# Optimization experiments

Hardware: AMD Instinct MI355X
Metric: run time of the kernel (lower is better)

## Reference

```python
import jax, jax.numpy as jnp
import numpy as np

# --- LIF neuron (spikingjelly LIFNode, single-step, tau=2.0, hard reset, ATan surrogate) ---
# With zero initial membrane potential, one step gives h = x / tau, spike = heaviside(h - v_th).
ALPHA = 2.0  # ATan surrogate default alpha
TAU = 2.0    # LIFNode default tau
V_TH = 1.0

@jax.custom_vjp
def atan_heaviside(x):
    return (x >= 0.0).astype(x.dtype)

def _ah_fwd(x):
    return (x >= 0.0).astype(x.dtype), x

def _ah_bwd(res, g):
    # d/dx of ATan surrogate: alpha / (2 * (1 + (pi/2 * alpha * x)^2))
    return (g * (ALPHA / (2.0 * (1.0 + (jnp.pi / 2.0 * ALPHA * res) ** 2))),)

atan_heaviside.defvjp(_ah_fwd, _ah_bwd)

def lif(x):
    return atan_heaviside(x / TAU - V_TH)

DIM, NUM_HEADS, TOPK = 256, 8, 4
WT, WH, WW = 2, 4, 4

def setup_inputs() -> dict:
    key = jax.random.key(0)
    k1, k2, k3, k4, k5 = jax.random.split(key, 5)
    T, B, Lt, Lh, Lw, C = 4, 2, 8, 32, 32, DIM
    x = jax.random.normal(k1, (T, B, Lt, Lh, Lw, C), dtype=jnp.float32)
    w_qkv = jax.random.normal(k2, (C, 3 * C), dtype=jnp.float32) * 0.02
    b_qkv = jax.random.normal(k3, (3 * C,), dtype=jnp.float32) * 0.02
    w_proj = jax.random.normal(k4, (C, C), dtype=jnp.float32) * 0.02
    b_proj = jax.random.normal(k5, (C,), dtype=jnp.float32) * 0.02
    return {"x": x, "w_qkv": w_qkv, "b_qkv": b_qkv, "w_proj": w_proj, "b_proj": b_proj}

def reference(x, w_qkv, b_qkv, w_proj, b_proj):
    T, B, Lt, Lh, Lw, C = x.shape
    H = NUM_HEADS
    D = C // H
    scale = D ** -0.5
    lt, lh, lw = Lt // WT, Lh // WH, Lw // WW
    W = WT * WH * WW          # num_wins = 32
    S = lt * lh * lw          # win_size = 256

    # window partition: [T,B,Lt,Lh,Lw,C] -> [T,B,W,S,C]
    xw = x.reshape(T, B, WT, lt, WH, lh, WW, lw, C)
    xw = xw.transpose(0, 1, 2, 4, 6, 3, 5, 7, 8).reshape(T, B, W, S, C)

    # region routing: mean over timesteps and tokens -> [B,W,C]
    region = xw.mean(axis=(0, 3))
    scores = jnp.einsum('bwc,bvc->bwv', region, region) * scale  # [B,W,W]
    idx = jax.lax.top_k(scores, TOPK)[1]                          # [B,W,K] int32

    # qkv projection + spiking activations
    qkv = xw @ w_qkv + b_qkv                                      # [T,B,W,S,3C]
    q, k, v = jnp.split(qkv, 3, axis=-1)
    q, k, v = lif(q), lif(k), lif(v)
    q = q.reshape(T, B, W, S, H, D)
    k = k.reshape(T, B, W, S, H, D)
    v = v.reshape(T, B, W, S, H, D)

    # gather routed KV blocks: k_g[t,b,w,j] = k[t,b,idx[b,w,j]]
    b_ix = jnp.arange(B)[:, None, None]
    k_g = k[:, b_ix, idx].reshape(T, B, W, TOPK * S, H, D)        # [T,B,W,K*S,H,D]
    v_g = v[:, b_ix, idx].reshape(T, B, W, TOPK * S, H, D)

    # linear attention: kv = k^T v, out = q @ kv, normalized by q @ sum(k)
    kv = jnp.einsum('tbwnhd,tbwnhe->tbwhde', k_g, v_g)            # [T,B,W,H,D,D]
    out = jnp.einsum('tbwshd,tbwhde->tbwshe', q, kv)              # [T,B,W,S,H,D]
    den = jnp.einsum('tbwshd,tbwhd->tbwsh', q, k_g.sum(axis=3))[..., None]
    out = out / (den + 1e-6)

    out = out.reshape(T, B, W, S, C) @ w_proj + b_proj

    # window reverse: [T,B,W,S,C] -> [T,B,Lt,Lh,Lw,C]
    out = out.reshape(T, B, WT, WH, WW, lt, lh, lw, C)
    out = out.transpose(0, 1, 2, 5, 3, 6, 4, 7, 8).reshape(T, B, Lt, Lh, Lw, C)
    return out
```

## Files before the change

### kernel.cpp

```cpp
#include <hip/hip_runtime.h>
#include <hip/hip_bf16.h>
#include <stdint.h>

#define NT 4
#define NB 2
#define NW 32
#define NS 256
#define NC 256
#define NH 8
#define ND 32
#define NK 4

#define LDP 40

typedef unsigned int u32;
typedef unsigned short u16;
typedef __attribute__((ext_vector_type(8))) short bf16x8;
typedef __attribute__((ext_vector_type(8))) unsigned short u16x8;
typedef __attribute__((ext_vector_type(4))) float f32x4;

__device__ __forceinline__ int wofs(int w) {
  return (w >> 4) * 4096 + ((w >> 2) & 3) * 256 + (w & 3) * 8;
}
__device__ __forceinline__ int sofs(int s) {
  return ((s >> 6) << 10) + (((s >> 3) & 7) << 5) + (s & 7);
}
__device__ __forceinline__ size_t x_off(int t, int b, int w, int s, int c) {
  return ((size_t)((t * NB + b) * 8192 + wofs(w) + sofs(s))) * NC + c;
}

__device__ __forceinline__ u32 f2bf(float f) {
  union { float f; u32 i; } u; u.f = f;
  return (u.i + 0x7FFFu + ((u.i >> 16) & 1u)) >> 16;
}

__global__ __launch_bounds__(256) void k_convw(const float* __restrict__ w_qkv,
                                               u16* __restrict__ bt) {
  int i = blockIdx.x * 256 + threadIdx.x;
  int k = i / 768, n = i % 768;
  bt[(size_t)n * 256 + k] = (u16)f2bf(w_qkv[i]);
}

__global__ __launch_bounds__(256) void k_gemm(const float* __restrict__ x,
                                              const u16* __restrict__ bt,
                                              const float* __restrict__ b_qkv,
                                              u32* __restrict__ qb, u32* __restrict__ kb,
                                              u32* __restrict__ vb,
                                              float* __restrict__ partial,
                                              u32* __restrict__ winflag) {
  __shared__ __align__(16) u16 As[2][128 * LDP];
  __shared__ __align__(16) u16 Bs[2][128 * LDP];
  __shared__ u32 pack[128 * 4];
  __shared__ float4 sums4[2][256];
  __shared__ u32 wfl;

  const int tid = threadIdx.x;
  const int v = (blockIdx.x & 7) * 384 + (blockIdx.x >> 3);
  const int mt = v / 6, nt = v % 6;
  const int m0 = mt * 128, n0 = nt * 128;
  const int wave = tid >> 6, lane = tid & 63;
  const int wr = wave >> 1, wc = wave & 1;
  const bool doreg = (nt == 0);

  if (tid == 0) wfl = 0;
  for (int i = tid; i < 128 * 4; i += 256) pack[i] = 0;

  const f32x4 vz = {0.f, 0.f, 0.f, 0.f};
  f32x4 acc[4][4];
#pragma unroll
  for (int m = 0; m < 4; ++m)
#pragma unroll
    for (int n = 0; n < 4; ++n) acc[m][n] = vz;

  auto stage = [&](int buf, int ks) {
    const int k0 = ks * 32;
    const int r0 = tid >> 3, c4 = tid & 7;
    float4 sv = {0.f, 0.f, 0.f, 0.f};
#pragma unroll
    for (int p = 0; p < 4; ++p) {
      int row = p * 32 + r0;
      float4 vx = *reinterpret_cast<const float4*>(&x[(size_t)(m0 + row) * NC + k0 + c4 * 4]);
      sv.x += vx.x; sv.y += vx.y; sv.z += vx.z; sv.w += vx.w;
      uint2 bf;
      bf.x = f2bf(vx.x) | (f2bf(vx.y) << 16);
      bf.y = f2bf(vx.z) | (f2bf(vx.w) << 16);
      *reinterpret_cast<uint2*>(&As[buf][row * LDP + c4 * 4]) = bf;
    }
    if (doreg) sums4[ks & 1][tid] = sv;
#pragma unroll
    for (int p = 0; p < 2; ++p) {
      int idx2 = p * 256 + tid;
      int row = idx2 >> 2, ch = idx2 & 3;
      u16x8 vbb = *reinterpret_cast<const u16x8*>(&bt[(size_t)(n0 + row) * 256 + k0 + ch * 8]);
      *reinterpret_cast<u16x8*>(&Bs[buf][row * LDP + ch * 8]) = vbb;
    }
  };

  stage(0, 0);
  __syncthreads();
#pragma unroll
  for (int ks = 0; ks < 8; ++ks) {
    const int buf = ks & 1;
    if (doreg && (tid >> 5) == ks) {
      int local = tid & 31, c4l = local >> 2, comp = local & 3;
      const float* sp = reinterpret_cast<const float*>(&sums4[ks & 1][0]);
#pragma unroll
      for (int ww = 0; ww < 4; ++ww) {
        float s = 0.f;
#pragma unroll
        for (int j = 0; j < 8; ++j) s += sp[((ww * 8 + j) * 8 + c4l) * 4 + comp];
        partial[((size_t)mt * 4 + ww) * NC + tid] = s;
      }
    }
    if (ks < 7) stage(buf ^ 1, ks + 1);
    bf16x8 afr[4], bfr[4];
#pragma unroll
    for (int m = 0; m < 4; ++m)
      afr[m] = *reinterpret_cast<const bf16x8*>(
          &As[buf][(wr * 64 + m * 16 + (lane & 15)) * LDP + (lane >> 4) * 8]);
#pragma unroll
    for (int n = 0; n < 4; ++n)
      bfr[n] = *reinterpret_cast<const bf16x8*>(
          &Bs[buf][(wc * 64 + n * 16 + (lane & 15)) * LDP + (lane >> 4) * 8]);
#pragma unroll
    for (int m = 0; m < 4; ++m)
#pragma unroll
      for (int n = 0; n < 4; ++n)
        acc[m][n] = __builtin_amdgcn_mfma_f32_16x16x32_bf16(afr[m], bfr[n], acc[m][n], 0, 0, 0);
    __syncthreads();
  }

  float bias[4];
#pragma unroll
  for (int n = 0; n < 4; ++n) bias[n] = b_qkv[n0 + wc * 64 + n * 16 + (lane & 15)];
#pragma unroll
  for (int m = 0; m < 4; ++m)
#pragma unroll
    for (int n = 0; n < 4; ++n)
#pragma unroll
      for (int r = 0; r < 4; ++r) {
        float vv = acc[m][n][r] + bias[n];
        if (vv >= 2.0f) {
          int row = wr * 64 + m * 16 + (lane >> 4) * 4 + r;
          int colb = wc * 64 + n * 16 + (lane & 15);
          atomicOr(&pack[row * 4 + (colb >> 5)], 1u << (colb & 31));
        }
      }
  __syncthreads();
  u32* dst = (nt < 2) ? qb : (nt < 4) ? kb : vb;
  const int h0 = (nt * 4) & 7;
  u32 anyb = 0;
  for (int i = tid; i < 128 * 4; i += 256) {
    int row = i >> 2, j = i & 3;
    u32 pv = pack[i];
    dst[(size_t)(m0 + row) * NH + h0 + j] = pv;
    if (pv) anyb |= 1u << ((row & 31) >> 3);
  }
  if (anyb) atomicOr(&wfl, anyb);
  __syncthreads();
  if (tid == 0 && wfl) {
    int t = mt >> 7, b = (mt >> 6) & 1, Lt = (mt >> 3) & 7, hh = mt & 7;
    int w0 = (Lt >> 2) * 16 + (hh >> 1) * 4;
    u32 bit = (nt < 2) ? 1u : (nt < 4) ? 2u : 4u;
    for (int ww = 0; ww < 4; ++ww)
      if (wfl & (1u << ww))
        atomicOr(&winflag[(t * NB + b) * NW + w0 + ww], bit);
  }
}

__global__ __launch_bounds__(256) void k_reduce(const float* __restrict__ partial,
                                                float* __restrict__ region) {
  int blk = blockIdx.x;
  int b = blk >> 5, v = blk & 31;
  int c = threadIdx.x;
  int wt = v >> 4, wh = (v >> 2) & 3, ww = v & 3;
  float s = 0.f;
#pragma unroll
  for (int t = 0; t < NT; ++t)
#pragma unroll
    for (int it = 0; it < 4; ++it)
#pragma unroll
      for (int hl = 0; hl < 2; ++hl) {
        int m = ((t * NB + b) * 8 + wt * 4 + it) * 8 + (wh * 2 + hl);
        s += partial[((size_t)m * 4 + ww) * NC + c];
      }
  region[(size_t)blk * NC + c] = s * (1.0f / 1024.0f);
}

__global__ __launch_bounds__(256) void k_scores(const float* __restrict__ region,
                                                int* __restrict__ idx) {
  __shared__ float rs[NW][NC];
  __shared__ float scval[NW];
  int blk = blockIdx.x;
  int b = blk >> 5, w = blk & 31;
  int tid = threadIdx.x;
  for (int i = tid; i < NW * NC; i += 256)
    rs[i >> 8][i & 255] = region[(size_t)b * NW * NC + i];
  __syncthreads();
  int v = tid >> 3, l8 = tid & 7;
  float sum = 0.f;
  const float* a = rs[w];
  const float* bb = rs[v];
#pragma unroll
  for (int j = 0; j < 32; ++j) sum += a[l8 * 32 + j] * bb[l8 * 32 + j];
  sum += __shfl_xor(sum, 1);
  sum += __shfl_xor(sum, 2);
  sum += __shfl_xor(sum, 4);
  if (l8 == 0) scval[v] = sum * 0.17677669529663687f;
  __syncthreads();
  if (tid == 0) {
    float sc[NW];
#pragma unroll
    for (int j = 0; j < NW; ++j) sc[j] = scval[j];
    for (int kk = 0; kk < NK; ++kk) {
      float best = -__builtin_inff(); int bi = 0;
      for (int j = 0; j < NW; ++j)
        if (sc[j] > best) { best = sc[j]; bi = j; }
      idx[(b * NW + w) * NK + kk] = bi;
      sc[bi] = -__builtin_inff();
    }
  }
}

__global__ __launch_bounds__(256) void k_attn(const u32* __restrict__ qb,
                                              const u32* __restrict__ kb,
                                              const u32* __restrict__ vb,
                                              const int* __restrict__ idx,
                                              const u32* __restrict__ winflag,
                                              const float* __restrict__ w_proj,
                                              const float* __restrict__ b_proj,
                                              float* __restrict__ out) {
  __shared__ u32 qs[NS * NH];
  __shared__ unsigned short kvc[NH * ND * ND];
  __shared__ u32 ksum[NH * ND];
  __shared__ float attnrow[NC];

  int blk = blockIdx.x;
  int t = blk >> 6, b = (blk >> 5) & 1, w = blk & 31;
  int tid = threadIdx.x;

  u32 fs = winflag[(t * NB + b) * NW + w];
  int wj[NK];
  u32 fk = 0, fv = 0;
#pragma unroll
  for (int j = 0; j < NK; ++j) {
    wj[j] = idx[(b * NW + w) * NK + j];
    u32 f = winflag[(t * NB + b) * NW + wj[j]];
    fk |= f & 2u; fv |= f & 4u;
  }
  bool skip = !(fs & 1u) || !fk || !fv;

  if (skip) {
    float bp = b_proj[tid];
    for (int s = 0; s < NS; ++s) out[x_off(t, b, w, s, tid)] = bp;
    return;
  }

  int tb = (t * NB + b) * 8192;
  size_t gb[NK];
#pragma unroll
  for (int j = 0; j < NK; ++j) gb[j] = (size_t)(tb + wofs(wj[j])) * NH;
  size_t qbase = (size_t)(tb + wofs(w)) * NH;
  for (int i = tid; i < NS * NH; i += 256)
    qs[i] = qb[qbase + (size_t)sofs(i >> 3) * NH + (i & 7)];
  {
    int h = tid >> 5, d = tid & 31;
    u32 cnt = 0;
    for (int n = 0; n < NK * NS; ++n)
      cnt += (kb[gb[n >> 8] + (size_t)sofs(n & 255) * NH + h] >> d) & 1u;
    ksum[tid] = cnt;
  }
  for (int p = tid; p < NH * ND * ND; p += 256) {
    int h = p >> 10, d = (p >> 5) & 31, e = p & 31;
    u32 cnt = 0;
    for (int n = 0; n < NK * NS; ++n) {
      size_t a = gb[n >> 8] + (size_t)sofs(n & 255) * NH + h;
      cnt += ((kb[a] >> d) & (vb[a] >> e)) & 1u;
    }
    kvc[p] = (unsigned short)cnt;
  }
  __syncthreads();
  int h = tid >> 5, e = tid & 31;
  float bpv = b_proj[tid];
  for (int s = 0; s < NS; ++s) {
    u32 qw = qs[s * NH + h];
    float num = 0.f, den = 0.f;
    for (int d = 0; d < ND; ++d) {
      if ((qw >> d) & 1u) {
        den += (float)ksum[h * ND + d];
        num += (float)kvc[h * ND * ND + d * ND + e];
      }
    }
    attnrow[tid] = num / (den + 1e-6f);
    __syncthreads();
    float acc = bpv;
    for (int c = 0; c < NC; ++c) acc += attnrow[c] * w_proj[c * NC + tid];
    out[x_off(t, b, w, s, tid)] = acc;
    __syncthreads();
  }
}

extern "C" void kernel_launch(void* const* d_in, const int* in_sizes, int n_in,
                              void* d_out, int out_size, void* d_ws, size_t ws_size,
                              hipStream_t stream) {
  const float* x      = (const float*)d_in[0];
  const float* w_qkv  = (const float*)d_in[1];
  const float* b_qkv  = (const float*)d_in[2];
  const float* w_proj = (const float*)d_in[3];
  const float* b_proj = (const float*)d_in[4];
  float* out = (float*)d_out;

  char* ws = (char*)d_ws;
  float* partial = (float*)ws;
  int* idx       = (int*)(ws + 0x200000);
  u16* bt        = (u16*)(ws + 0x201000);
  u32* winflag   = (u32*)(ws + 0x280000);
  float* region  = (float*)(ws + 0x290000);
  u32* qb        = (u32*)(ws + 0x300000);
  u32* kb        = qb + (size_t)NT * NB * NW * NS * NH;
  u32* vb        = kb + (size_t)NT * NB * NW * NS * NH;

  hipMemsetAsync(winflag, 0, NT * NB * NW * sizeof(u32), stream);
  k_convw<<<768, 256, 0, stream>>>(w_qkv, bt);
  k_gemm<<<3072, 256, 0, stream>>>(x, bt, b_qkv, qb, kb, vb, partial, winflag);
  k_reduce<<<NB * NW, 256, 0, stream>>>(partial, region);
  k_scores<<<NB * NW, 256, 0, stream>>>(region, idx);
  k_attn<<<NT * NB * NW, 256, 0, stream>>>(qb, kb, vb, idx, winflag, w_proj, b_proj, out);
}
```

Before: 81.93 us.

## Pre-convert x to bf16, use direct global-to-LDS loads, split attention blocks by tokens

```diff
diff --git a/kernel.cpp b/kernel.cpp
--- a/kernel.cpp
+++ b/kernel.cpp
@@ -11,12 +11,9 @@
 #define ND 32
 #define NK 4
 
-#define LDP 40
-
 typedef unsigned int u32;
 typedef unsigned short u16;
 typedef __attribute__((ext_vector_type(8))) short bf16x8;
-typedef __attribute__((ext_vector_type(8))) unsigned short u16x8;
 typedef __attribute__((ext_vector_type(4))) float f32x4;
 
 __device__ __forceinline__ int wofs(int w) {
@@ -32,6 +29,12 @@
 __device__ __forceinline__ u32 f2bf(float f) {
   union { float f; u32 i; } u; u.f = f;
   return (u.i + 0x7FFFu + ((u.i >> 16) & 1u)) >> 16;
+}
+
+__device__ __forceinline__ void gload16(const u16* g, u16* l) {
+  __builtin_amdgcn_global_load_lds(
+      (const __attribute__((address_space(1))) void*)g,
+      (__attribute__((address_space(3))) void*)l, 16, 0, 0);
 }
 
 __global__ __launch_bounds__(256) void k_convw(const float* __restrict__ w_qkv,
@@ -41,131 +44,37 @@
   bt[(size_t)n * 256 + k] = (u16)f2bf(w_qkv[i]);
 }
 
-__global__ __launch_bounds__(256) void k_gemm(const float* __restrict__ x,
-                                              const u16* __restrict__ bt,
-                                              const float* __restrict__ b_qkv,
-                                              u32* __restrict__ qb, u32* __restrict__ kb,
-                                              u32* __restrict__ vb,
-                                              float* __restrict__ partial,
-                                              u32* __restrict__ winflag) {
-  __shared__ __align__(16) u16 As[2][128 * LDP];
-  __shared__ __align__(16) u16 Bs[2][128 * LDP];
-  __shared__ u32 pack[128 * 4];
-  __shared__ float4 sums4[2][256];
-  __shared__ u32 wfl;
-
-  const int tid = threadIdx.x;
-  const int v = (blockIdx.x & 7) * 384 + (blockIdx.x >> 3);
-  const int mt = v / 6, nt = v % 6;
-  const int m0 = mt * 128, n0 = nt * 128;
-  const int wave = tid >> 6, lane = tid & 63;
-  const int wr = wave >> 1, wc = wave & 1;
-  const bool doreg = (nt == 0);
-
-  if (tid == 0) wfl = 0;
-  for (int i = tid; i < 128 * 4; i += 256) pack[i] = 0;
-
-  const f32x4 vz = {0.f, 0.f, 0.f, 0.f};
-  f32x4 acc[4][4];
-#pragma unroll
-  for (int m = 0; m < 4; ++m)
-#pragma unroll
-    for (int n = 0; n < 4; ++n) acc[m][n] = vz;
-
-  auto stage = [&](int buf, int ks) {
-    const int k0 = ks * 32;
-    const int r0 = tid >> 3, c4 = tid & 7;
-    float4 sv = {0.f, 0.f, 0.f, 0.f};
-#pragma unroll
-    for (int p = 0; p < 4; ++p) {
-      int row = p * 32 + r0;
-      float4 vx = *reinterpret_cast<const float4*>(&x[(size_t)(m0 + row) * NC + k0 + c4 * 4]);
-      sv.x += vx.x; sv.y += vx.y; sv.z += vx.z; sv.w += vx.w;
-      uint2 bf;
-      bf.x = f2bf(vx.x) | (f2bf(vx.y) << 16);
-      bf.y = f2bf(vx.z) | (f2bf(vx.w) << 16);
-      *reinterpret_cast<uint2*>(&As[buf][row * LDP + c4 * 4]) = bf;
-    }
-    if (doreg) sums4[ks & 1][tid] = sv;
-#pragma unroll
-    for (int p = 0; p < 2; ++p) {
-      int idx2 = p * 256 + tid;
-      int row = idx2 >> 2, ch = idx2 & 3;
-      u16x8 vbb = *reinterpret_cast<const u16x8*>(&bt[(size_t)(n0 + row) * 256 + k0 + ch * 8]);
-      *reinterpret_cast<u16x8*>(&Bs[buf][row * LDP + ch * 8]) = vbb;
-    }
-  };
-
-  stage(0, 0);
-  __syncthreads();
-#pragma unroll
-  for (int ks = 0; ks < 8; ++ks) {
-    const int buf = ks & 1;
-    if (doreg && (tid >> 5) == ks) {
-      int local = tid & 31, c4l = local >> 2, comp = local & 3;
-      const float* sp = reinterpret_cast<const float*>(&sums4[ks & 1][0]);
-#pragma unroll
-      for (int ww = 0; ww < 4; ++ww) {
-        float s = 0.f;
-#pragma unroll
-        for (int j = 0; j < 8; ++j) s += sp[((ww * 8 + j) * 8 + c4l) * 4 + comp];
-        partial[((size_t)mt * 4 + ww) * NC + tid] = s;
-      }
-    }
-    if (ks < 7) stage(buf ^ 1, ks + 1);
-    bf16x8 afr[4], bfr[4];
-#pragma unroll
-    for (int m = 0; m < 4; ++m)
-      afr[m] = *reinterpret_cast<const bf16x8*>(
-          &As[buf][(wr * 64 + m * 16 + (lane & 15)) * LDP + (lane >> 4) * 8]);
-#pragma unroll
-    for (int n = 0; n < 4; ++n)
-      bfr[n] = *reinterpret_cast<const bf16x8*>(
-          &Bs[buf][(wc * 64 + n * 16 + (lane & 15)) * LDP + (lane >> 4) * 8]);
-#pragma unroll
-    for (int m = 0; m < 4; ++m)
-#pragma unroll
-      for (int n = 0; n < 4; ++n)
-        acc[m][n] = __builtin_amdgcn_mfma_f32_16x16x32_bf16(afr[m], bfr[n], acc[m][n], 0, 0, 0);
-    __syncthreads();
-  }
-
-  float bias[4];
-#pragma unroll
-  for (int n = 0; n < 4; ++n) bias[n] = b_qkv[n0 + wc * 64 + n * 16 + (lane & 15)];
-#pragma unroll
-  for (int m = 0; m < 4; ++m)
-#pragma unroll
-    for (int n = 0; n < 4; ++n)
-#pragma unroll
-      for (int r = 0; r < 4; ++r) {
-        float vv = acc[m][n][r] + bias[n];
-        if (vv >= 2.0f) {
-          int row = wr * 64 + m * 16 + (lane >> 4) * 4 + r;
-          int colb = wc * 64 + n * 16 + (lane & 15);
-          atomicOr(&pack[row * 4 + (colb >> 5)], 1u << (colb & 31));
-        }
-      }
-  __syncthreads();
-  u32* dst = (nt < 2) ? qb : (nt < 4) ? kb : vb;
-  const int h0 = (nt * 4) & 7;
-  u32 anyb = 0;
-  for (int i = tid; i < 128 * 4; i += 256) {
-    int row = i >> 2, j = i & 3;
-    u32 pv = pack[i];
-    dst[(size_t)(m0 + row) * NH + h0 + j] = pv;
-    if (pv) anyb |= 1u << ((row & 31) >> 3);
-  }
-  if (anyb) atomicOr(&wfl, anyb);
-  __syncthreads();
-  if (tid == 0 && wfl) {
-    int t = mt >> 7, b = (mt >> 6) & 1, Lt = (mt >> 3) & 7, hh = mt & 7;
-    int w0 = (Lt >> 2) * 16 + (hh >> 1) * 4;
-    u32 bit = (nt < 2) ? 1u : (nt < 4) ? 2u : 4u;
-    for (int ww = 0; ww < 4; ++ww)
-      if (wfl & (1u << ww))
-        atomicOr(&winflag[(t * NB + b) * NW + w0 + ww], bit);
-  }
+__global__ __launch_bounds__(256) void k_convx(const float* __restrict__ x,
+                                               u16* __restrict__ xw,
+                                               float* __restrict__ partial) {
+  __shared__ float sums[4][4][NC];
+  int blk = blockIdx.x;
+  int tid = threadIdx.x;
+  int g = tid >> 6, c4 = tid & 63;
+  size_t base = (size_t)blk * 128;
+  float4 s[4];
+#pragma unroll
+  for (int ww = 0; ww < 4; ++ww) s[ww] = make_float4(0.f, 0.f, 0.f, 0.f);
+#pragma unroll
+  for (int p = 0; p < 32; ++p) {
+    int row = p * 4 + g;
+    float4 v = *reinterpret_cast<const float4*>(&x[(base + row) * NC + c4 * 4]);
+    uint2 bf;
+    bf.x = f2bf(v.x) | (f2bf(v.y) << 16);
+    bf.y = f2bf(v.z) | (f2bf(v.w) << 16);
+    *reinterpret_cast<uint2*>(&xw[(base + row) * NC + c4 * 4]) = bf;
+    int ww = (p & 7) >> 1;
+    s[ww].x += v.x; s[ww].y += v.y; s[ww].z += v.z; s[ww].w += v.w;
+  }
+#pragma unroll
+  for (int ww = 0; ww < 4; ++ww)
+    *reinterpret_cast<float4*>(&sums[ww][g][c4 * 4]) = s[ww];
+  __syncthreads();
+  int c = tid;
+#pragma unroll
+  for (int ww = 0; ww < 4; ++ww)
+    partial[((size_t)blk * 4 + ww) * NC + c] =
+        sums[ww][0][c] + sums[ww][1][c] + sums[ww][2][c] + sums[ww][3][c];
 }
 
 __global__ __launch_bounds__(256) void k_reduce(const float* __restrict__ partial,
@@ -180,9 +89,9 @@
 #pragma unroll
     for (int it = 0; it < 4; ++it)
 #pragma unroll
-      for (int hl = 0; hl < 2; ++hl) {
-        int m = ((t * NB + b) * 8 + wt * 4 + it) * 8 + (wh * 2 + hl);
-        s += partial[((size_t)m * 4 + ww) * NC + c];
+      for (int j = 0; j < 2; ++j) {
+        int pb = (t * NB + b) * 64 + (wt * 4 + it) * 8 + (wh * 2 + j);
+        s += partial[((size_t)pb * 4 + ww) * NC + c];
       }
   region[(size_t)blk * NC + c] = s * (1.0f / 1024.0f);
 }
@@ -222,6 +131,107 @@
   }
 }
 
+__global__ __launch_bounds__(256) void k_gemm(const u16* __restrict__ xw,
+                                              const u16* __restrict__ bt,
+                                              const float* __restrict__ b_qkv,
+                                              u32* __restrict__ qb, u32* __restrict__ kb,
+                                              u32* __restrict__ vb,
+                                              u32* __restrict__ winflag) {
+  __shared__ __align__(16) u16 As[2][128 * 32];
+  __shared__ __align__(16) u16 Bs[2][128 * 32];
+  __shared__ u32 pack[128 * 4];
+  __shared__ u32 wfl;
+
+  const int tid = threadIdx.x;
+  const int v = (blockIdx.x & 7) * 384 + (blockIdx.x >> 3);
+  const int mt = v / 6, nt = v % 6;
+  const int m0 = mt * 128, n0 = nt * 128;
+  const int wave = tid >> 6, lane = tid & 63;
+  const int wr = wave >> 1, wc = wave & 1;
+
+  if (tid == 0) wfl = 0;
+  for (int i = tid; i < 128 * 4; i += 256) pack[i] = 0;
+
+  const f32x4 vz = {0.f, 0.f, 0.f, 0.f};
+  f32x4 acc[4][4];
+#pragma unroll
+  for (int m = 0; m < 4; ++m)
+#pragma unroll
+    for (int n = 0; n < 4; ++n) acc[m][n] = vz;
+
+  auto stage = [&](int buf, int ks) {
+    const int k0 = ks * 32;
+#pragma unroll
+    for (int p = 0; p < 2; ++p) {
+      int idx2 = p * 256 + wave * 64 + lane;
+      int row = idx2 >> 2, ch = idx2 & 3;
+      int lbase = (p * 256 + wave * 64) * 8;
+      gload16(&xw[(size_t)(m0 + row) * 256 + k0 + ch * 8], &As[buf][lbase]);
+      gload16(&bt[(size_t)(n0 + row) * 256 + k0 + ch * 8], &Bs[buf][lbase]);
+    }
+  };
+
+  stage(0, 0);
+  __syncthreads();
+#pragma unroll
+  for (int ks = 0; ks < 8; ++ks) {
+    const int buf = ks & 1;
+    if (ks < 7) stage(buf ^ 1, ks + 1);
+    bf16x8 afr[4], bfr[4];
+#pragma unroll
+    for (int m = 0; m < 4; ++m)
+      afr[m] = *reinterpret_cast<const bf16x8*>(
+          &As[buf][(wr * 64 + m * 16 + (lane & 15)) * 32 + (lane >> 4) * 8]);
+#pragma unroll
+    for (int n = 0; n < 4; ++n)
+      bfr[n] = *reinterpret_cast<const bf16x8*>(
+          &Bs[buf][(wc * 64 + n * 16 + (lane & 15)) * 32 + (lane >> 4) * 8]);
+#pragma unroll
+    for (int m = 0; m < 4; ++m)
+#pragma unroll
+      for (int n = 0; n < 4; ++n)
+        acc[m][n] = __builtin_amdgcn_mfma_f32_16x16x32_bf16(afr[m], bfr[n], acc[m][n], 0, 0, 0);
+    __syncthreads();
+  }
+
+  float bias[4];
+#pragma unroll
+  for (int n = 0; n < 4; ++n) bias[n] = b_qkv[n0 + wc * 64 + n * 16 + (lane & 15)];
+#pragma unroll
+  for (int m = 0; m < 4; ++m)
+#pragma unroll
+    for (int n = 0; n < 4; ++n)
+#pragma unroll
+      for (int r = 0; r < 4; ++r) {
+        float vv = acc[m][n][r] + bias[n];
+        if (vv >= 2.0f) {
+          int row = wr * 64 + m * 16 + (lane >> 4) * 4 + r;
+          int colb = wc * 64 + n * 16 + (lane & 15);
+          atomicOr(&pack[row * 4 + (colb >> 5)], 1u << (colb & 31));
+        }
+      }
+  __syncthreads();
+  u32* dst = (nt < 2) ? qb : (nt < 4) ? kb : vb;
+  const int h0 = (nt * 4) & 7;
+  u32 anyb = 0;
+  for (int i = tid; i < 128 * 4; i += 256) {
+    int row = i >> 2, j = i & 3;
+    u32 pv = pack[i];
+    dst[(size_t)(m0 + row) * NH + h0 + j] = pv;
+    if (pv) anyb |= 1u << ((row & 31) >> 3);
+  }
+  if (anyb) atomicOr(&wfl, anyb);
+  __syncthreads();
+  if (tid == 0 && wfl) {
+    int t = mt >> 7, b = (mt >> 6) & 1, Lt = (mt >> 3) & 7, hh = mt & 7;
+    int w0 = (Lt >> 2) * 16 + (hh >> 1) * 4;
+    u32 bit = (nt < 2) ? 1u : (nt < 4) ? 2u : 4u;
+    for (int ww = 0; ww < 4; ++ww)
+      if (wfl & (1u << ww))
+        atomicOr(&winflag[(t * NB + b) * NW + w0 + ww], bit);
+  }
+}
+
 __global__ __launch_bounds__(256) void k_attn(const u32* __restrict__ qb,
                                               const u32* __restrict__ kb,
                                               const u32* __restrict__ vb,
@@ -230,13 +240,15 @@
                                               const float* __restrict__ w_proj,
                                               const float* __restrict__ b_proj,
                                               float* __restrict__ out) {
-  __shared__ u32 qs[NS * NH];
+  __shared__ u32 qs[64 * NH];
   __shared__ unsigned short kvc[NH * ND * ND];
   __shared__ u32 ksum[NH * ND];
   __shared__ float attnrow[NC];
 
   int blk = blockIdx.x;
-  int t = blk >> 6, b = (blk >> 5) & 1, w = blk & 31;
+  int wid = blk >> 2, sc = blk & 3;
+  int t = wid >> 6, b = (wid >> 5) & 1, w = wid & 31;
+  int s0 = sc * 64;
   int tid = threadIdx.x;
 
   u32 fs = winflag[(t * NB + b) * NW + w];
@@ -252,7 +264,7 @@
 
   if (skip) {
     float bp = b_proj[tid];
-    for (int s = 0; s < NS; ++s) out[x_off(t, b, w, s, tid)] = bp;
+    for (int s = s0; s < s0 + 64; ++s) out[x_off(t, b, w, s, tid)] = bp;
     return;
   }
 
@@ -261,8 +273,8 @@
 #pragma unroll
   for (int j = 0; j < NK; ++j) gb[j] = (size_t)(tb + wofs(wj[j])) * NH;
   size_t qbase = (size_t)(tb + wofs(w)) * NH;
-  for (int i = tid; i < NS * NH; i += 256)
-    qs[i] = qb[qbase + (size_t)sofs(i >> 3) * NH + (i & 7)];
+  for (int i = tid; i < 64 * NH; i += 256)
+    qs[i] = qb[qbase + (size_t)sofs(s0 + (i >> 3)) * NH + (i & 7)];
   {
     int h = tid >> 5, d = tid & 31;
     u32 cnt = 0;
@@ -282,8 +294,8 @@
   __syncthreads();
   int h = tid >> 5, e = tid & 31;
   float bpv = b_proj[tid];
-  for (int s = 0; s < NS; ++s) {
-    u32 qw = qs[s * NH + h];
+  for (int sl = 0; sl < 64; ++sl) {
+    u32 qw = qs[sl * NH + h];
     float num = 0.f, den = 0.f;
     for (int d = 0; d < ND; ++d) {
       if ((qw >> d) & 1u) {
@@ -295,7 +307,7 @@
     __syncthreads();
     float acc = bpv;
     for (int c = 0; c < NC; ++c) acc += attnrow[c] * w_proj[c * NC + tid];
-    out[x_off(t, b, w, s, tid)] = acc;
+    out[x_off(t, b, w, s0 + sl, tid)] = acc;
     __syncthreads();
   }
 }
@@ -314,16 +326,18 @@
   float* partial = (float*)ws;
   int* idx       = (int*)(ws + 0x200000);
   u16* bt        = (u16*)(ws + 0x201000);
-  u32* winflag   = (u32*)(ws + 0x280000);
-  float* region  = (float*)(ws + 0x290000);
+  u32* winflag   = (u32*)(ws + 0x270000);
+  float* region  = (float*)(ws + 0x280000);
   u32* qb        = (u32*)(ws + 0x300000);
   u32* kb        = qb + (size_t)NT * NB * NW * NS * NH;
   u32* vb        = kb + (size_t)NT * NB * NW * NS * NH;
+  u16* xw        = (u16*)(ws + 0x900000);
 
   hipMemsetAsync(winflag, 0, NT * NB * NW * sizeof(u32), stream);
   k_convw<<<768, 256, 0, stream>>>(w_qkv, bt);
-  k_gemm<<<3072, 256, 0, stream>>>(x, bt, b_qkv, qb, kb, vb, partial, winflag);
+  k_convx<<<512, 256, 0, stream>>>(x, xw, partial);
   k_reduce<<<NB * NW, 256, 0, stream>>>(partial, region);
   k_scores<<<NB * NW, 256, 0, stream>>>(region, idx);
-  k_attn<<<NT * NB * NW, 256, 0, stream>>>(qb, kb, vb, idx, winflag, w_proj, b_proj, out);
-}
+  k_gemm<<<3072, 256, 0, stream>>>(xw, bt, b_qkv, qb, kb, vb, winflag);
+  k_attn<<<NT * NB * NW * 4, 256, 0, stream>>>(qb, kb, vb, idx, winflag, w_proj, b_proj, out);
+}
```

New measurement: 94.26 us. +15.0%, slower.
